# Kernel optimization log

Hardware: AMD Instinct MI355X
Metric: run time of the kernel (lower is better)

Reference implementation:

```python
import jax, jax.numpy as jnp
import numpy as np

B, I, C, J, D, H, W = 16, 32, 8, 10, 16, 6, 6
NUM_ROUTING = 3
EPS = 1e-07


def setup_inputs() -> dict:
    key = jax.random.key(0)
    u_hat = jax.random.normal(key, (B, I, C, J, D, H, W), dtype=jnp.float32)
    # torch module fills bias with 0.1, shape (out_capsules, out_channels, 1, 1)
    bias = jnp.full((J, D, 1, 1), 0.1, dtype=jnp.float32)
    return {"u_hat": u_hat, "bias": bias, "num_routing": NUM_ROUTING}


def _squash(s):
    # Faithful to the source: L1 norm over ALL non-batch dims (not per-capsule L2).
    n1 = jnp.sum(jnp.abs(s), axis=(1, 2, 3, 4), keepdims=True)  # [B,1,1,1,1]
    n1_sq = n1 * n1
    return (n1_sq / (1.0 + n1_sq)) * (s / (n1 + EPS))


def reference(u_hat, bias, num_routing):
    # u_hat: [B,I,C,J,D,H,W]; bias: [J,D,1,1]
    b_ij = jnp.zeros((I, J), dtype=u_hat.dtype)
    v_j = None
    for _ in range(num_routing):
        c_ij = jax.nn.softmax(b_ij, axis=1)  # [I,J]
        # s_j[b,j,d,h,w] = sum_{i,c} c[i,j] * u_hat[b,i,c,j,d,h,w]  (c broadcast over in_channels)
        s_j = jnp.einsum('ij,bicjdhw->bjdhw', c_ij, u_hat) + bias
        v_j = _squash(s_j)  # [B,J,D,H,W]
        # agreement[i,j] = sum over b,c,d,h,w of u_hat * v_j (broadcast over i,c)
        agreement = jnp.einsum('bicjdhw,bjdhw->ij', u_hat, v_j)
        b_ij = b_ij + jax.lax.stop_gradient(agreement)  # torch uses .data (detached)
    return v_j
```

## Files before the change

### kernel.cpp

```cpp
#include <hip/hip_runtime.h>


#define NB   16
#define NI   32
#define NC   8
#define NJ   10
#define ND   16
#define NHW  36
#define NDHW 576
#define NBJ  (NB * NJ)
#define NJDHW (NJ * NDHW)
#define NTOT  (NB * NJ * NDHW)
#define EPSV 1e-7f
#define TPB  576

static __device__ __forceinline__ double wave_sum(double v) {
    #pragma unroll
    for (int off = 32; off > 0; off >>= 1) v += __shfl_down(v, off);
    return v;
}

static __device__ __forceinline__ void n1_reduce(float sv, double* slot,
                                                 double* nred ) {
    int tid = threadIdx.x;
    double a = wave_sum((double)fabsf(sv));
    if ((tid & 63) == 0) nred[tid >> 6] = a;
    __syncthreads();
    if (tid == 0) {
        double t = nred[0];
        #pragma unroll
        for (int w = 1; w < 9; ++w) t += nred[w];
        *slot = t;
    }
}

static __device__ __forceinline__ void g_reduce(const float* Uv, float sv,
                                                double* gslot,
                                                double (*gred)[32] ) {
    int tid = threadIdx.x, w = tid >> 6, lane = tid & 63;
    #pragma unroll
    for (int i = 0; i < NI; ++i) {
        double p = wave_sum((double)Uv[i] * (double)sv);
        if (lane == 0) gred[w][i] = p;
    }
    __syncthreads();
    if (tid < NI) {
        double t = gred[0][tid];
        #pragma unroll
        for (int w2 = 1; w2 < 9; ++w2) t += gred[w2][tid];
        gslot[tid] = t;
    }
}

static __device__ __forceinline__ void grid_barrier(unsigned* bar) {
    __syncthreads();
    if (threadIdx.x == 0) {
        __threadfence();
        unsigned g = __hip_atomic_load(&bar[1], __ATOMIC_RELAXED,
                                       __HIP_MEMORY_SCOPE_AGENT);
        unsigned a = __hip_atomic_fetch_add(&bar[0], 1u, __ATOMIC_RELAXED,
                                            __HIP_MEMORY_SCOPE_AGENT);
        if (a == (unsigned)(NBJ - 1)) {
            __hip_atomic_store(&bar[0], 0u, __ATOMIC_RELAXED,
                               __HIP_MEMORY_SCOPE_AGENT);
            __hip_atomic_fetch_add(&bar[1], 1u, __ATOMIC_RELEASE,
                                   __HIP_MEMORY_SCOPE_AGENT);
        } else {
            int guard = 0;
            while (__hip_atomic_load(&bar[1], __ATOMIC_RELAXED,
                                     __HIP_MEMORY_SCOPE_AGENT) == g) {
                __builtin_amdgcn_s_sleep(8);
                if (++guard > (1 << 17)) break;
            }
        }
        __threadfence();
    }
    __syncthreads();
}

__global__ void init_bar(unsigned* bar) {
    if (threadIdx.x < 2) bar[threadIdx.x] = 0u;
}

__global__ __launch_bounds__(TPB) void fused_kernel(
    const float4* __restrict__ uh4, const float* __restrict__ bias,
    double* __restrict__ n1p, double* __restrict__ Gp,
    unsigned* __restrict__ bar, float* __restrict__ out)
{
    __shared__ float4  Utile4[NI * 144];
    __shared__ double  nred[9];
    __shared__ double  gred[9][32];
    __shared__ double  sc_sh[2][NB];
    __shared__ float   bij_sh[NI * NJ];
    __shared__ float   c_sh[NI];

    const int blk = blockIdx.x;
    const int b = blk / NJ, j = blk - b * NJ;
    const int tid = threadIdx.x;

    #pragma unroll
    for (int g = 0; g < 8; ++g) {
        int lin = g * TPB + tid;
        int i  = lin / 144, f4 = lin - i * 144;
        const float4* p = uh4 + ((size_t)(b * NI + i) * NC) * 1440 + j * 144 + f4;
        float4 acc = make_float4(0.f, 0.f, 0.f, 0.f);
        #pragma unroll
        for (int c = 0; c < NC; ++c) {
            float4 v = p[(size_t)c * 1440];
            acc.x += v.x; acc.y += v.y; acc.z += v.z; acc.w += v.w;
        }
        Utile4[lin] = acc;
    }
    __syncthreads();

    const float* Utile = (const float*)Utile4;
    float Uv[NI];
    #pragma unroll
    for (int i = 0; i < NI; ++i) Uv[i] = Utile[i * NDHW + tid];
    const float bv = bias[j * ND + tid / NHW];

    const float cw = 1.0f / 10.0f;
    float sv = bv;
    #pragma unroll
    for (int i = 0; i < NI; ++i) sv += cw * Uv[i];

    n1_reduce(sv, &n1p[blk], nred);
    g_reduce(Uv, sv, &Gp[(size_t)blk * NI], gred);
    grid_barrier(bar);

    for (int R = 1; R <= 2; ++R) {
        if (tid < R * NB) {
            int rr = tid / NB, bb = tid - rr * NB;
            double n1 = 0.0;
            #pragma unroll
            for (int jj = 0; jj < NJ; ++jj) n1 += n1p[rr * NBJ + bb * NJ + jj];
            double nsq = n1 * n1;
            sc_sh[rr][bb] = (nsq / (1.0 + nsq)) / (n1 + (double)EPSV);
        }
        __syncthreads();

        if (tid < NI * NJ) {
            int i = tid / NJ, jj = tid - i * NJ;
            double a = 0.0;
            for (int rr = 0; rr < R; ++rr)
                #pragma unroll
                for (int bb = 0; bb < NB; ++bb)
                    a += sc_sh[rr][bb] *
                         Gp[(size_t)(rr * NB + bb) * (NJ * NI) + (size_t)jj * NI + i];
            bij_sh[tid] = (float)a;
        }
        __syncthreads();

        if (tid < NI) {
            float m = -1e30f;
            #pragma unroll
            for (int jj = 0; jj < NJ; ++jj) m = fmaxf(m, bij_sh[tid * NJ + jj]);
            float sum = 0.f;
            #pragma unroll
            for (int jj = 0; jj < NJ; ++jj) sum += expf(bij_sh[tid * NJ + jj] - m);
            c_sh[tid] = expf(bij_sh[tid * NJ + j] - m) / sum;
        }
        __syncthreads();

        sv = bv;
        #pragma unroll
        for (int i = 0; i < NI; ++i) sv += c_sh[i] * Uv[i];

        n1_reduce(sv, &n1p[R * NBJ + blk], nred);
        if (R == 1)
            g_reduce(Uv, sv, &Gp[(size_t)(NBJ + blk) * NI], gred);
        grid_barrier(bar);
    }

    if (tid == 0) {
        double n1 = 0.0;
        #pragma unroll
        for (int jj = 0; jj < NJ; ++jj) n1 += n1p[2 * NBJ + b * NJ + jj];
        nred[0] = n1;
    }
    __syncthreads();
    float n1f = (float)nred[0];
    float nsq = n1f * n1f;
    out[(size_t)blk * NDHW + tid] = (nsq / (1.f + nsq)) * (sv / (n1f + EPSV));
}

extern "C" void kernel_launch(void* const* d_in, const int* in_sizes, int n_in,
                              void* d_out, int out_size, void* d_ws, size_t ws_size,
                              hipStream_t stream)
{
    const float* u_hat = (const float*)d_in[0];
    const float* bias  = (const float*)d_in[1];
    float* out = (float*)d_out;

    double*   n1p = (double*)d_ws;
    double*   Gp  = n1p + 3 * NBJ;
    unsigned* bar = (unsigned*)(Gp + 2 * NBJ * NI);

    init_bar<<<1, 64, 0, stream>>>(bar);
    fused_kernel<<<NBJ, TPB, 0, stream>>>(
        (const float4*)u_hat, bias, n1p, Gp, bar, out);
}
```

Before: 216.1 us.

## Split each (b,j) block into three chunks with atomic G reduction and tree barrier

```diff
diff --git a/kernel.cpp b/kernel.cpp
--- a/kernel.cpp
+++ b/kernel.cpp
@@ -8,11 +8,16 @@
 #define ND   16
 #define NHW  36
 #define NDHW 576
+#define CK   3
+#define CHK  192
 #define NBJ  (NB * NJ)
-#define NJDHW (NJ * NDHW)
+#define NBJC (NBJ * CK)
 #define NTOT  (NB * NJ * NDHW)
 #define EPSV 1e-7f
-#define TPB  576
+#define TPB  192
+#define NLEAF 8
+#define PER_LEAF (NBJC / NLEAF)
+#define BAR_U32 (NLEAF * 32 + 64)
 
 static __device__ __forceinline__ double wave_sum(double v) {
     #pragma unroll
@@ -26,17 +31,12 @@
     double a = wave_sum((double)fabsf(sv));
     if ((tid & 63) == 0) nred[tid >> 6] = a;
     __syncthreads();
-    if (tid == 0) {
-        double t = nred[0];
-        #pragma unroll
-        for (int w = 1; w < 9; ++w) t += nred[w];
-        *slot = t;
-    }
-}
-
-static __device__ __forceinline__ void g_reduce(const float* Uv, float sv,
-                                                double* gslot,
-                                                double (*gred)[32] ) {
+    if (tid == 0) slot[0] = (nred[0] + nred[1]) + nred[2];
+}
+
+static __device__ __forceinline__ void g_reduce_atomic(const float* Uv, float sv,
+                                                       double* gslot,
+                                                       double (*gred)[32]) {
     int tid = threadIdx.x, w = tid >> 6, lane = tid & 63;
     #pragma unroll
     for (int i = 0; i < NI; ++i) {
@@ -44,65 +44,74 @@
         if (lane == 0) gred[w][i] = p;
     }
     __syncthreads();
-    if (tid < NI) {
-        double t = gred[0][tid];
-        #pragma unroll
-        for (int w2 = 1; w2 < 9; ++w2) t += gred[w2][tid];
-        gslot[tid] = t;
-    }
+    if (tid < NI)
+        atomicAdd(&gslot[tid], (gred[0][tid] + gred[1][tid]) + gred[2][tid]);
 }
 
 static __device__ __forceinline__ void grid_barrier(unsigned* bar) {
     __syncthreads();
     if (threadIdx.x == 0) {
         __threadfence();
-        unsigned g = __hip_atomic_load(&bar[1], __ATOMIC_RELAXED,
+        unsigned* leaf = &bar[(blockIdx.x & (NLEAF - 1)) * 32];
+        unsigned* root = &bar[NLEAF * 32];
+        unsigned* gen  = &bar[NLEAF * 32 + 32];
+        unsigned g = __hip_atomic_load(gen, __ATOMIC_RELAXED,
                                        __HIP_MEMORY_SCOPE_AGENT);
-        unsigned a = __hip_atomic_fetch_add(&bar[0], 1u, __ATOMIC_RELAXED,
+        unsigned a = __hip_atomic_fetch_add(leaf, 1u, __ATOMIC_ACQ_REL,
                                             __HIP_MEMORY_SCOPE_AGENT);
-        if (a == (unsigned)(NBJ - 1)) {
-            __hip_atomic_store(&bar[0], 0u, __ATOMIC_RELAXED,
+        if (a == PER_LEAF - 1) {
+            __hip_atomic_store(leaf, 0u, __ATOMIC_RELAXED,
                                __HIP_MEMORY_SCOPE_AGENT);
-            __hip_atomic_fetch_add(&bar[1], 1u, __ATOMIC_RELEASE,
+            unsigned r = __hip_atomic_fetch_add(root, 1u, __ATOMIC_ACQ_REL,
+                                                __HIP_MEMORY_SCOPE_AGENT);
+            if (r == NLEAF - 1) {
+                __hip_atomic_store(root, 0u, __ATOMIC_RELAXED,
                                    __HIP_MEMORY_SCOPE_AGENT);
-        } else {
-            int guard = 0;
-            while (__hip_atomic_load(&bar[1], __ATOMIC_RELAXED,
-                                     __HIP_MEMORY_SCOPE_AGENT) == g) {
-                __builtin_amdgcn_s_sleep(8);
-                if (++guard > (1 << 17)) break;
+                __hip_atomic_fetch_add(gen, 1u, __ATOMIC_RELEASE,
+                                       __HIP_MEMORY_SCOPE_AGENT);
             }
         }
+        int guard = 0;
+        while (__hip_atomic_load(gen, __ATOMIC_RELAXED,
+                                 __HIP_MEMORY_SCOPE_AGENT) == g) {
+            __builtin_amdgcn_s_sleep(8);
+            if (++guard > (1 << 17)) break;
+        }
         __threadfence();
     }
     __syncthreads();
 }
 
-__global__ void init_bar(unsigned* bar) {
-    if (threadIdx.x < 2) bar[threadIdx.x] = 0u;
+__global__ __launch_bounds__(256) void init_kernel(double* __restrict__ AGp,
+                                                   unsigned* __restrict__ bar) {
+    int idx = blockIdx.x * 256 + threadIdx.x;
+    if (idx < 2 * NBJ * NI) AGp[idx] = 0.0;
+    if (idx < BAR_U32) bar[idx] = 0u;
 }
 
 __global__ __launch_bounds__(TPB) void fused_kernel(
     const float4* __restrict__ uh4, const float* __restrict__ bias,
-    double* __restrict__ n1p, double* __restrict__ Gp,
+    double* __restrict__ n1p, double* __restrict__ AGp,
     unsigned* __restrict__ bar, float* __restrict__ out)
 {
-    __shared__ float4  Utile4[NI * 144];
-    __shared__ double  nred[9];
-    __shared__ double  gred[9][32];
+    __shared__ float4  Utile4[NI * 48];
+    __shared__ double  nred[3];
+    __shared__ double  gred[3][32];
     __shared__ double  sc_sh[2][NB];
     __shared__ float   bij_sh[NI * NJ];
     __shared__ float   c_sh[NI];
 
     const int blk = blockIdx.x;
-    const int b = blk / NJ, j = blk - b * NJ;
+    const int bj = blk / CK, ck = blk - bj * CK;
+    const int b = bj / NJ,  j  = bj - b * NJ;
     const int tid = threadIdx.x;
 
     #pragma unroll
     for (int g = 0; g < 8; ++g) {
         int lin = g * TPB + tid;
-        int i  = lin / 144, f4 = lin - i * 144;
-        const float4* p = uh4 + ((size_t)(b * NI + i) * NC) * 1440 + j * 144 + f4;
+        int i  = lin / 48, f4 = lin - i * 48;
+        const float4* p = uh4 + ((size_t)(b * NI + i) * NC) * 1440
+                              + j * 144 + ck * 48 + f4;
         float4 acc = make_float4(0.f, 0.f, 0.f, 0.f);
         #pragma unroll
         for (int c = 0; c < NC; ++c) {
@@ -116,8 +125,8 @@
     const float* Utile = (const float*)Utile4;
     float Uv[NI];
     #pragma unroll
-    for (int i = 0; i < NI; ++i) Uv[i] = Utile[i * NDHW + tid];
-    const float bv = bias[j * ND + tid / NHW];
+    for (int i = 0; i < NI; ++i) Uv[i] = Utile[i * CHK + tid];
+    const float bv = bias[j * ND + (ck * CHK + tid) / NHW];
 
     const float cw = 1.0f / 10.0f;
     float sv = bv;
@@ -125,7 +134,7 @@
     for (int i = 0; i < NI; ++i) sv += cw * Uv[i];
 
     n1_reduce(sv, &n1p[blk], nred);
-    g_reduce(Uv, sv, &Gp[(size_t)blk * NI], gred);
+    g_reduce_atomic(Uv, sv, &AGp[(size_t)bj * NI], gred);
     grid_barrier(bar);
 
     for (int R = 1; R <= 2; ++R) {
@@ -133,21 +142,25 @@
             int rr = tid / NB, bb = tid - rr * NB;
             double n1 = 0.0;
             #pragma unroll
-            for (int jj = 0; jj < NJ; ++jj) n1 += n1p[rr * NBJ + bb * NJ + jj];
+            for (int jj = 0; jj < NJ; ++jj)
+                #pragma unroll
+                for (int cc = 0; cc < CK; ++cc)
+                    n1 += n1p[(size_t)rr * NBJC + (bb * NJ + jj) * CK + cc];
             double nsq = n1 * n1;
             sc_sh[rr][bb] = (nsq / (1.0 + nsq)) / (n1 + (double)EPSV);
         }
         __syncthreads();
 
-        if (tid < NI * NJ) {
-            int i = tid / NJ, jj = tid - i * NJ;
+        for (int e = tid; e < NI * NJ; e += TPB) {
+            int i = e / NJ, jj = e - i * NJ;
             double a = 0.0;
             for (int rr = 0; rr < R; ++rr)
                 #pragma unroll
                 for (int bb = 0; bb < NB; ++bb)
                     a += sc_sh[rr][bb] *
-                         Gp[(size_t)(rr * NB + bb) * (NJ * NI) + (size_t)jj * NI + i];
-            bij_sh[tid] = (float)a;
+                         AGp[(size_t)rr * (NBJ * NI) +
+                             (size_t)(bb * NJ + jj) * NI + i];
+            bij_sh[e] = (float)a;
         }
         __syncthreads();
 
@@ -166,22 +179,26 @@
         #pragma unroll
         for (int i = 0; i < NI; ++i) sv += c_sh[i] * Uv[i];
 
-        n1_reduce(sv, &n1p[R * NBJ + blk], nred);
+        n1_reduce(sv, &n1p[(size_t)R * NBJC + blk], nred);
         if (R == 1)
-            g_reduce(Uv, sv, &Gp[(size_t)(NBJ + blk) * NI], gred);
+            g_reduce_atomic(Uv, sv, &AGp[(size_t)(NBJ + bj) * NI], gred);
         grid_barrier(bar);
     }
 
     if (tid == 0) {
         double n1 = 0.0;
         #pragma unroll
-        for (int jj = 0; jj < NJ; ++jj) n1 += n1p[2 * NBJ + b * NJ + jj];
+        for (int jj = 0; jj < NJ; ++jj)
+            #pragma unroll
+            for (int cc = 0; cc < CK; ++cc)
+                n1 += n1p[(size_t)2 * NBJC + (b * NJ + jj) * CK + cc];
         nred[0] = n1;
     }
     __syncthreads();
     float n1f = (float)nred[0];
     float nsq = n1f * n1f;
-    out[(size_t)blk * NDHW + tid] = (nsq / (1.f + nsq)) * (sv / (n1f + EPSV));
+    out[(size_t)bj * NDHW + ck * CHK + tid] =
+        (nsq / (1.f + nsq)) * (sv / (n1f + EPSV));
 }
 
 extern "C" void kernel_launch(void* const* d_in, const int* in_sizes, int n_in,
@@ -193,10 +210,10 @@
     float* out = (float*)d_out;
 
     double*   n1p = (double*)d_ws;
-    double*   Gp  = n1p + 3 * NBJ;
-    unsigned* bar = (unsigned*)(Gp + 2 * NBJ * NI);
-
-    init_bar<<<1, 64, 0, stream>>>(bar);
-    fused_kernel<<<NBJ, TPB, 0, stream>>>(
-        (const float4*)u_hat, bias, n1p, Gp, bar, out);
-}
+    double*   AGp = n1p + 3 * NBJC;
+    unsigned* bar = (unsigned*)(AGp + 2 * NBJ * NI);
+
+    init_kernel<<<(2 * NBJ * NI + 255) / 256, 256, 0, stream>>>(AGp, bar);
+    fused_kernel<<<NBJC, TPB, 0, stream>>>(
+        (const float4*)u_hat, bias, n1p, AGp, bar, out);
+}
```

New measurement: 231.6 us. 7.2% more time.
